# Optimization experiments

Hardware: AMD Instinct MI355X
Metric: run time of the kernel (lower is better)

Reference implementation:

```python
import jax, jax.numpy as jnp
import numpy as np

N_HEAD = 16
D_HEAD = 64
D_MODEL = 1024
SCALE = 1.0 / float(D_HEAD) ** 0.5
LN_EPS = 1e-5


def _rel_shift(x):
    # x: [b, n, i, j] -> Transformer-XL relative shift
    b, n, i, j = x.shape
    x = jnp.pad(x, ((0, 0), (0, 0), (0, 0), (1, 0)))  # zero-pad front of last dim
    x = x.reshape(b, n, j + 1, i)[:, :, 1:, :]
    return x.reshape(b, n, i, j)


def _layer_norm(x, g, b):
    mu = jnp.mean(x, axis=-1, keepdims=True)
    var = jnp.mean(jnp.square(x - mu), axis=-1, keepdims=True)
    return g * (x - mu) / jnp.sqrt(var + LN_EPS) + b


def setup_inputs() -> dict:
    key = jax.random.key(0)
    ks = jax.random.split(key, 8)
    qlen, bsz = 1024, 4
    w = jax.random.normal(ks[0], (qlen, bsz, D_MODEL), jnp.float32)
    r = jax.random.normal(ks[1], (qlen, D_MODEL), jnp.float32)
    r_w_bias = 0.02 * jax.random.normal(ks[2], (N_HEAD, D_HEAD), jnp.float32)
    r_r_bias = 0.02 * jax.random.normal(ks[3], (N_HEAD, D_HEAD), jnp.float32)
    attn_mask = jnp.triu(jnp.ones((qlen, qlen), bool), 1)  # causal, True = masked
    qkv_w = 0.02 * jax.random.normal(ks[4], (D_MODEL, 3 * N_HEAD * D_HEAD), jnp.float32)
    qkv_b = jnp.zeros((3 * N_HEAD * D_HEAD,), jnp.float32)
    rk_w = 0.02 * jax.random.normal(ks[5], (D_MODEL, N_HEAD * D_HEAD), jnp.float32)
    rk_b = jnp.zeros((N_HEAD * D_HEAD,), jnp.float32)
    o_w = 0.02 * jax.random.normal(ks[6], (N_HEAD * D_HEAD, D_MODEL), jnp.float32)
    o_b = jnp.zeros((D_MODEL,), jnp.float32)
    ln_g = jnp.ones((D_MODEL,), jnp.float32)
    ln_b = jnp.zeros((D_MODEL,), jnp.float32)
    return {"w": w, "r": r, "r_w_bias": r_w_bias, "r_r_bias": r_r_bias,
            "qkv_w": qkv_w, "qkv_b": qkv_b, "rk_w": rk_w, "rk_b": rk_b,
            "o_w": o_w, "o_b": o_b, "ln_g": ln_g, "ln_b": ln_b,
            "attn_mask": attn_mask}


def reference(w, r, r_w_bias, r_r_bias, qkv_w, qkv_b, rk_w, rk_b, o_w, o_b, ln_g, ln_b, attn_mask):
    qlen, bsz, _ = w.shape
    # post-lnorm path (pre_lnorm=False)
    heads = w @ qkv_w + qkv_b                       # [q, b, 3*H*D]
    q, k, v = jnp.split(heads, 3, axis=-1)
    q = q.reshape(qlen, bsz, N_HEAD, D_HEAD)
    k = k.reshape(qlen, bsz, N_HEAD, D_HEAD)
    v = v.reshape(qlen, bsz, N_HEAD, D_HEAD)
    rk = (r @ rk_w + rk_b).reshape(-1, N_HEAD, D_HEAD)  # [rlen, H, D]
    AC = jnp.einsum('ibnd,jbnd->bnij', q + r_w_bias, k)
    BD = _rel_shift(jnp.einsum('ibnd,jnd->bnij', q + r_r_bias, rk))
    score = SCALE * (AC + BD)                       # [b, H, q, k]
    score = jnp.where(attn_mask[None, None, :, :], -jnp.inf, score)
    prob = jax.nn.softmax(score, axis=-1)
    vec = jnp.einsum('bnij,jbnd->ibnd', prob, v).reshape(qlen, bsz, N_HEAD * D_HEAD)
    attn_out = vec @ o_w + o_b
    return _layer_norm(w + attn_out, ln_g, ln_b)
```

## Files before the change

### kernel.cpp

```cpp
#include <hip/hip_runtime.h>
#include <math.h>

#define QL 1024
#define BSZ 4
#define NH 16
#define DH 64
#define DM 1024
#define SCALE_F 0.125f

typedef __attribute__((ext_vector_type(8))) short bf16x8;
typedef __attribute__((ext_vector_type(4))) float f32x4;

__device__ __forceinline__ unsigned short f2bf(float f) {
  union { float f; unsigned int u; } c; c.f = f;
  unsigned int u = c.u;
  u += 0x7FFFu + ((u >> 16) & 1u);
  return (unsigned short)(u >> 16);
}
__device__ __forceinline__ float bf2f(unsigned short u) {
  union { unsigned int i; float f; } c; c.i = ((unsigned int)u) << 16;
  return c.f;
}
__device__ __forceinline__ float2 bfp2f(const unsigned short* p) {
  unsigned int u = *(const unsigned int*)p;
  union { unsigned int u; float f; } lo, hi;
  lo.u = (u & 0xFFFFu) << 16;
  hi.u = u & 0xFFFF0000u;
  return make_float2(lo.f, hi.f);
}

__device__ __forceinline__ void ld_lds16(const unsigned short* g, unsigned short* l) {
  __builtin_amdgcn_global_load_lds(
      (const __attribute__((address_space(1))) unsigned int*)g,
      (__attribute__((address_space(3))) unsigned int*)l, 16, 0, 0);
}

__device__ __forceinline__ bf16x8 frag64(const unsigned short* lds, int n, int s) {
  return *(const bf16x8*)(lds + n * 64 + ((s ^ (n & 7)) * 8));
}

__global__ __launch_bounds__(256) void prep_kernel(
    const float* __restrict__ w, const float* __restrict__ r,
    const float* __restrict__ qkv_w, const float* __restrict__ rk_w,
    const float* __restrict__ o_w,
    unsigned short* __restrict__ wb, unsigned short* __restrict__ rb,
    unsigned short* __restrict__ qkv_wt, unsigned short* __restrict__ rk_wt,
    unsigned short* __restrict__ o_wt) {
  __shared__ __align__(16) unsigned short t[64][72];
  const int bid = blockIdx.x, tid = threadIdx.x;
  if (bid < 2560) {
    const float* in = (bid < 2048) ? w : r;
    unsigned short* out = (bid < 2048) ? wb : rb;
    int idx = ((bid < 2048) ? bid : (bid - 2048)) * 256 + tid;
    float4 a = *(const float4*)(in + (size_t)idx * 8);
    float4 b = *(const float4*)(in + (size_t)idx * 8 + 4);
    unsigned short o[8] = {f2bf(a.x), f2bf(a.y), f2bf(a.z), f2bf(a.w),
                           f2bf(b.x), f2bf(b.y), f2bf(b.z), f2bf(b.w)};
    *(uint4*)(out + (size_t)idx * 8) = *(const uint4*)o;
    return;
  }
  const float* in; unsigned short* out; int N, n0, k0;
  if (bid < 3328) {
    int l = bid - 2560; in = qkv_w; out = qkv_wt; N = 3072;
    n0 = (l % 48) * 64; k0 = (l / 48) * 64;
  } else if (bid < 3584) {
    int l = bid - 3328; in = rk_w; out = rk_wt; N = 1024;
    n0 = (l & 15) * 64; k0 = (l >> 4) * 64;
  } else {
    int l = bid - 3584; in = o_w; out = o_wt; N = 1024;
    n0 = (l & 15) * 64; k0 = (l >> 4) * 64;
  }
  for (int f = tid; f < 1024; f += 256) {
    int rr = f >> 4, c4 = (f & 15) * 4;
    float4 v = *(const float4*)(in + (size_t)(k0 + rr) * N + n0 + c4);
    t[c4 + 0][rr] = f2bf(v.x); t[c4 + 1][rr] = f2bf(v.y);
    t[c4 + 2][rr] = f2bf(v.z); t[c4 + 3][rr] = f2bf(v.w);
  }
  __syncthreads();
  for (int f = tid; f < 512; f += 256) {
    int rr = f >> 3, seg = (f & 7) * 8;
    *(uint4*)(out + (size_t)(n0 + rr) * 1024 + k0 + seg) = *(const uint4*)&t[rr][seg];
  }
}

__global__ __launch_bounds__(512) void gemm12(
    const unsigned short* __restrict__ wb, const unsigned short* __restrict__ rb,
    const unsigned short* __restrict__ qkv_wt, const unsigned short* __restrict__ rk_wt,
    const float* __restrict__ qkv_b, const float* __restrict__ rk_b,
    const float* __restrict__ rwb, const float* __restrict__ rrb,
    unsigned short* __restrict__ qbf, unsigned short* __restrict__ kbf,
    unsigned short* __restrict__ vtb, unsigned short* __restrict__ rkbf,
    float* __restrict__ drk) {
  __shared__ __align__(16) unsigned short As[2 * 4096];
  __shared__ __align__(16) unsigned short Bs[2 * 4096];
  const int bid = blockIdx.x, tid = threadIdx.x;
  const int w = tid >> 6, lane = tid & 63;
  const int quad = lane >> 4, l15 = lane & 15;
  const int wr = w >> 2, wc = w & 3;
  const bool job0 = bid < 768;
  const unsigned short *A, *BT;
  const float* bias;
  int bm, bn;
  if (job0) {
    A = wb; BT = qkv_wt; bias = qkv_b;
    bn = (bid % 24) * 128; bm = (bid / 24) * 128;
  } else {
    int l = bid - 768;
    A = rb; BT = rk_wt; bias = rk_b;
    bn = (l & 7) * 128; bm = (l >> 3) * 128;
  }
  const int srow = w * 16 + (lane >> 2);
  const int sseg = (lane & 3) ^ ((lane >> 2) & 3);
  f32x4 acc[4][2] = {};

  auto stage = [&](int bf, int k0) {
    ld_lds16(A + (size_t)(bm + srow) * 1024 + k0 + sseg * 8, As + bf * 4096 + w * 512);
    ld_lds16(BT + (size_t)(bn + srow) * 1024 + k0 + sseg * 8, Bs + bf * 4096 + w * 512);
  };

  int buf = 0;
  stage(0, 0);
  for (int k0 = 0; k0 < 1024; k0 += 32) {
    __syncthreads();
    if (k0 + 32 < 1024) stage(buf ^ 1, k0 + 32);
    const unsigned short* Al = As + buf * 4096;
    const unsigned short* Bl = Bs + buf * 4096;
    const int sa = quad ^ (l15 & 3);
    bf16x8 af[4], bfr[2];
#pragma unroll
    for (int rt = 0; rt < 4; ++rt)
      af[rt] = *(const bf16x8*)&Al[(wr * 64 + rt * 16 + l15) * 32 + sa * 8];
#pragma unroll
    for (int nt = 0; nt < 2; ++nt)
      bfr[nt] = *(const bf16x8*)&Bl[(wc * 32 + nt * 16 + l15) * 32 + sa * 8];
#pragma unroll
    for (int rt = 0; rt < 4; ++rt)
#pragma unroll
      for (int nt = 0; nt < 2; ++nt)
        acc[rt][nt] = __builtin_amdgcn_mfma_f32_16x16x32_bf16(af[rt], bfr[nt], acc[rt][nt], 0, 0, 0);
    buf ^= 1;
  }

  if (job0) {
#pragma unroll
    for (int rt = 0; rt < 4; ++rt)
#pragma unroll
      for (int nt = 0; nt < 2; ++nt) {
        int gc = bn + wc * 32 + nt * 16 + l15;
        float bv = bias[gc];
        int part = gc >> 10, h = (gc >> 6) & 15, d = gc & 63;
#pragma unroll
        for (int reg = 0; reg < 4; ++reg) {
          int gr = bm + wr * 64 + rt * 16 + quad * 4 + reg;
          float val = acc[rt][nt][reg] + bv;
          int i = gr >> 2, b = gr & 3;
          if (part == 0)
            qbf[((size_t)((b * NH + h) * QL + i)) * DH + d] = f2bf(val);
          else if (part == 1)
            kbf[((size_t)((b * NH + h) * QL + i)) * DH + d] = f2bf(val);
          else
            vtb[((size_t)((b * NH + h) * DH + d)) * QL + i] = f2bf(val);
        }
      }
  } else {
    const int h = (bn + wc * 32) >> 6;
    float df[2];
#pragma unroll
    for (int nt = 0; nt < 2; ++nt) {
      int dd = (wc & 1) * 32 + nt * 16 + l15;
      df[nt] = rrb[h * DH + dd] - rwb[h * DH + dd];
    }
#pragma unroll
    for (int rt = 0; rt < 4; ++rt) {
      float s[4] = {0.f, 0.f, 0.f, 0.f};
#pragma unroll
      for (int nt = 0; nt < 2; ++nt) {
        int gc = bn + wc * 32 + nt * 16 + l15;
        float bv = bias[gc];
        int d = gc & 63;
#pragma unroll
        for (int reg = 0; reg < 4; ++reg) {
          int gr = bm + wr * 64 + rt * 16 + quad * 4 + reg;
          float val = acc[rt][nt][reg] + bv;
          rkbf[((size_t)(h * QL + gr)) * DH + d] = f2bf(val);
          s[reg] += val * df[nt];
        }
      }
#pragma unroll
      for (int reg = 0; reg < 4; ++reg) {
        float v = s[reg];
        v += __shfl_xor(v, 1);
        v += __shfl_xor(v, 2);
        v += __shfl_xor(v, 4);
        v += __shfl_xor(v, 8);
        if (l15 == 0) {
          int j = bm + wr * 64 + rt * 16 + quad * 4 + reg;
          atomicAdd(&drk[h * QL + j], v);
        }
      }
    }
  }
}

__global__ __launch_bounds__(512) void gemm_o(
    const unsigned short* __restrict__ A, const unsigned short* __restrict__ BT,
    const float* __restrict__ bias, float* __restrict__ Cf) {
  __shared__ __align__(16) unsigned short As[2 * 4096];
  __shared__ __align__(16) unsigned short Bs[2 * 4096];
  const int tid = threadIdx.x;
  const int w = tid >> 6, lane = tid & 63;
  const int quad = lane >> 4, l15 = lane & 15;
  const int wr = w >> 2, wc = w & 3;
  const int bm = blockIdx.y * 128, bn = blockIdx.x * 128;
  const int srow = w * 16 + (lane >> 2);
  const int sseg = (lane & 3) ^ ((lane >> 2) & 3);
  f32x4 acc[4][2] = {};

  auto stage = [&](int bf, int k0) {
    ld_lds16(A + (size_t)(bm + srow) * 1024 + k0 + sseg * 8, As + bf * 4096 + w * 512);
    ld_lds16(BT + (size_t)(bn + srow) * 1024 + k0 + sseg * 8, Bs + bf * 4096 + w * 512);
  };

  int buf = 0;
  stage(0, 0);
  for (int k0 = 0; k0 < 1024; k0 += 32) {
    __syncthreads();
    if (k0 + 32 < 1024) stage(buf ^ 1, k0 + 32);
    const unsigned short* Al = As + buf * 4096;
    const unsigned short* Bl = Bs + buf * 4096;
    const int sa = quad ^ (l15 & 3);
    bf16x8 af[4], bfr[2];
#pragma unroll
    for (int rt = 0; rt < 4; ++rt)
      af[rt] = *(const bf16x8*)&Al[(wr * 64 + rt * 16 + l15) * 32 + sa * 8];
#pragma unroll
    for (int nt = 0; nt < 2; ++nt)
      bfr[nt] = *(const bf16x8*)&Bl[(wc * 32 + nt * 16 + l15) * 32 + sa * 8];
#pragma unroll
    for (int rt = 0; rt < 4; ++rt)
#pragma unroll
      for (int nt = 0; nt < 2; ++nt)
        acc[rt][nt] = __builtin_amdgcn_mfma_f32_16x16x32_bf16(af[rt], bfr[nt], acc[rt][nt], 0, 0, 0);
    buf ^= 1;
  }

#pragma unroll
  for (int rt = 0; rt < 4; ++rt)
#pragma unroll
    for (int nt = 0; nt < 2; ++nt) {
      int gc = bn + wc * 32 + nt * 16 + l15;
      float bv = bias[gc];
#pragma unroll
      for (int reg = 0; reg < 4; ++reg) {
        int gr = bm + wr * 64 + rt * 16 + quad * 4 + reg;
        Cf[(size_t)gr * DM + gc] = acc[rt][nt][reg] + bv;
      }
    }
}

__global__ __launch_bounds__(256) void attn_kernel(
    const unsigned short* __restrict__ qbf, const unsigned short* __restrict__ kbf,
    const unsigned short* __restrict__ vtb, const unsigned short* __restrict__ rkb,
    const float* __restrict__ drk, const float* __restrict__ rwb,
    unsigned short* __restrict__ vecb) {
  __shared__ __align__(16) unsigned short ks[2 * 4096];
  __shared__ __align__(16) unsigned short vt[2 * 4096];
  __shared__ __align__(16) unsigned short band[2][4096];

  const int tid = threadIdx.x;
  const int w = tid >> 6, lane = tid & 63;
  const int quad = lane >> 4, l15 = lane & 15;
  const int bh = blockIdx.x, b = bh >> 4, h = bh & 15;
  const int yA = blockIdx.y;
  const int i0A = yA * 64, i0B = (15 - yA) * 64;
  const int tA = yA, tB = 15 - yA;

  const unsigned short* kB0 = kbf + (size_t)bh * QL * DH;
  const unsigned short* vB0 = vtb + (size_t)bh * DH * QL;
  const unsigned short* rB0 = rkb + (size_t)h * QL * DH;
  const float* drkh = drk + h * QL;

  const int srow = lane >> 3, sseg = lane & 7;
  auto stage_tile = [&](const unsigned short* gbase, size_t rstride, unsigned short* lds) {
#pragma unroll
    for (int ii = 0; ii < 2; ++ii) {
      int r = ii * 32 + w * 8 + srow;
      int gseg = sseg ^ (r & 7);
      ld_lds16(gbase + (size_t)r * rstride + gseg * 8, lds + ii * 2048 + w * 512);
    }
  };

  auto load_q = [&](int i0, bf16x8* qf) {
    int qrow = i0 + w * 16 + l15;
    const unsigned short* qp = qbf + ((size_t)bh * QL + qrow) * DH;
#pragma unroll
    for (int s = 0; s < 2; ++s) {
      int off = s * 32 + quad * 8;
      uint4 raw = *(const uint4*)(qp + off);
      const unsigned short* ru = (const unsigned short*)&raw;
      float4 wb0 = *(const float4*)(rwb + h * DH + off);
      float4 wb1 = *(const float4*)(rwb + h * DH + off + 4);
      union { bf16x8 v; unsigned short u[8]; } qc;
      qc.u[0] = f2bf(bf2f(ru[0]) + wb0.x); qc.u[1] = f2bf(bf2f(ru[1]) + wb0.y);
      qc.u[2] = f2bf(bf2f(ru[2]) + wb0.z); qc.u[3] = f2bf(bf2f(ru[3]) + wb0.w);
      qc.u[4] = f2bf(bf2f(ru[4]) + wb1.x); qc.u[5] = f2bf(bf2f(ru[5]) + wb1.y);
      qc.u[6] = f2bf(bf2f(ru[6]) + wb1.z); qc.u[7] = f2bf(bf2f(ru[7]) + wb1.w);
      qf[s] = qc.v;
    }
  };
  bf16x8 qfA[2], qfB[2];
  load_q(i0A, qfA);
  load_q(i0B, qfB);

  auto rel_frag = [&](int gb, const bf16x8* qf, f32x4& c, float& dv) {
    int gc = min(gb + l15, QL - 1);
    const unsigned short* rp = rB0 + (size_t)gc * DH;
    f32x4 a = {0.f, 0.f, 0.f, 0.f};
    a = __builtin_amdgcn_mfma_f32_16x16x32_bf16(qf[0], *(const bf16x8*)(rp + quad * 8), a, 0, 0, 0);
    a = __builtin_amdgcn_mfma_f32_16x16x32_bf16(qf[1], *(const bf16x8*)(rp + 32 + quad * 8), a, 0, 0, 0);
    c = a;
    dv = drkh[gc];
  };

  stage_tile(kB0, DH, ks);
  stage_tile(vB0, QL, vt);

  f32x4 raccA[5], raccB[5];
  float dvA[5], dvB[5];
#pragma unroll
  for (int i = 0; i < 5; ++i) {
    rel_frag(1008 - i0A - 16 * w + 16 * i, qfA, raccA[i], dvA[i]);
    rel_frag(1008 - i0B - 16 * w + 16 * i, qfB, raccB[i], dvB[i]);
  }

  float mA[4], lA[4], mB[4], lB[4];
  f32x4 pvA[4], pvB[4];
#pragma unroll
  for (int r = 0; r < 4; ++r) {
    mA[r] = mB[r] = -1e30f; lA[r] = lB[r] = 0.f;
    pvA[r] = pvB[r] = (f32x4){0.f, 0.f, 0.f, 0.f};
  }

  auto do_stream = [&](const bf16x8* qf, f32x4* racc, float* dv, float* mrow, float* lrow,
                       f32x4* pv, bool diag, const unsigned short* ksl,
                       const unsigned short* vtl, unsigned short* bandS) {
    f32x4 sacc[4];
#pragma unroll
    for (int nt = 0; nt < 4; ++nt) {
      int n = nt * 16 + l15;
      f32x4 c = {0.f, 0.f, 0.f, 0.f};
      c = __builtin_amdgcn_mfma_f32_16x16x32_bf16(qf[0], frag64(ksl, n, quad), c, 0, 0, 0);
      c = __builtin_amdgcn_mfma_f32_16x16x32_bf16(qf[1], frag64(ksl, n, 4 + quad), c, 0, 0, 0);
      sacc[nt] = c;
    }
#pragma unroll
    for (int i = 0; i < 5; ++i) {
      float dvv = dv[i];
#pragma unroll
      for (int r = 0; r < 4; ++r) {
        int c = 16 * i + l15 + 4 * quad + r - 15;
        int il = w * 16 + quad * 4 + r;
        if (c >= 0 && c < 64)
          bandS[il * 64 + (c ^ ((il & 7) << 3))] = f2bf(racc[i][r] + dvv);
      }
    }
#pragma unroll
    for (int r = 0; r < 4; ++r) {
      const int il = w * 16 + quad * 4 + r;
      const int sw = (il & 7) << 3;
      float sv[4], smax = -1e30f;
#pragma unroll
      for (int nt = 0; nt < 4; ++nt) {
        int jl = nt * 16 + l15;
        float s = (sacc[nt][r] + bf2f(bandS[il * 64 + (jl ^ sw)])) * SCALE_F;
        if (diag && jl > il) s = -1e30f;
        sv[nt] = s;
        smax = fmaxf(smax, s);
      }
      smax = fmaxf(smax, __shfl_xor(smax, 1));
      smax = fmaxf(smax, __shfl_xor(smax, 2));
      smax = fmaxf(smax, __shfl_xor(smax, 4));
      smax = fmaxf(smax, __shfl_xor(smax, 8));
      float mnew = fmaxf(mrow[r], smax);
      float alpha = __expf(mrow[r] - mnew);
      mrow[r] = mnew;
      float psum = 0.f;
#pragma unroll
      for (int nt = 0; nt < 4; ++nt) {
        float e = __expf(sv[nt] - mnew);
        bandS[il * 64 + ((nt * 16 + l15) ^ sw)] = f2bf(e);
        psum += e;
      }
      psum += __shfl_xor(psum, 1);
      psum += __shfl_xor(psum, 2);
      psum += __shfl_xor(psum, 4);
      psum += __shfl_xor(psum, 8);
      lrow[r] = lrow[r] * alpha + psum;
#pragma unroll
      for (int nt = 0; nt < 4; ++nt) pv[nt][r] *= alpha;
    }
    {
      const int ilr = w * 16 + l15;
      const int swr = ilr & 7;
      bf16x8 pf0 = *(const bf16x8*)&bandS[ilr * 64 + ((quad ^ swr) * 8)];
      bf16x8 pf1 = *(const bf16x8*)&bandS[ilr * 64 + (((4 + quad) ^ swr) * 8)];
#pragma unroll
      for (int nt = 0; nt < 4; ++nt) {
        int n = nt * 16 + l15;
        pv[nt] = __builtin_amdgcn_mfma_f32_16x16x32_bf16(pf0, frag64(vtl, n, quad), pv[nt], 0, 0, 0);
        pv[nt] = __builtin_amdgcn_mfma_f32_16x16x32_bf16(pf1, frag64(vtl, n, 4 + quad), pv[nt], 0, 0, 0);
      }
    }
  };

  int buf = 0;
  for (int t = 0; t <= tB; ++t) {
    __syncthreads();
    if (t < tB) {
      int j1 = (t + 1) << 6;
      stage_tile(kB0 + (size_t)j1 * DH, DH, ks + (buf ^ 1) * 4096);
      stage_tile(vB0 + j1, QL, vt + (buf ^ 1) * 4096);
    }
    const unsigned short* ksl = ks + buf * 4096;
    const unsigned short* vtl = vt + buf * 4096;
    const bool actA = (t <= tA);

    if (t > 0) {
      raccB[0] = raccB[4]; dvB[0] = dvB[4];
      const int GB = 1008 - i0B + 64 * t - 16 * w;
#pragma unroll
      for (int i = 1; i < 5; ++i) rel_frag(GB + 16 * i, qfB, raccB[i], dvB[i]);
      if (actA) {
        raccA[0] = raccA[4]; dvA[0] = dvA[4];
        const int GA = 1008 - i0A + 64 * t - 16 * w;
#pragma unroll
        for (int i = 1; i < 5; ++i) rel_frag(GA + 16 * i, qfA, raccA[i], dvA[i]);
      }
    }

    do_stream(qfB, raccB, dvB, mB, lB, pvB, t == tB, ksl, vtl, band[1]);
    if (actA)
      do_stream(qfA, raccA, dvA, mA, lA, pvA, t == tA, ksl, vtl, band[0]);
    buf ^= 1;
  }

#pragma unroll
  for (int nt = 0; nt < 4; ++nt)
#pragma unroll
    for (int reg = 0; reg < 4; ++reg) {
      int il = w * 16 + quad * 4 + reg;
      int d = nt * 16 + l15;
      vecb[((size_t)((i0A + il) * BSZ + b)) * DM + h * DH + d] = f2bf(pvA[nt][reg] / lA[reg]);
      vecb[((size_t)((i0B + il) * BSZ + b)) * DM + h * DH + d] = f2bf(pvB[nt][reg] / lB[reg]);
    }
}

__global__ __launch_bounds__(256) void ln_kernel(
    const float* __restrict__ w, const float* __restrict__ attn,
    const float* __restrict__ g, const float* __restrict__ bta,
    float* __restrict__ out) {
  __shared__ float red[4];
  __shared__ float sval[2];
  const int row = blockIdx.x, tid = threadIdx.x;
  const float* wr = w + (size_t)row * DM;
  const float* ar = attn + (size_t)row * DM;
  float4 wv = *(const float4*)(wr + tid * 4);
  float4 av = *(const float4*)(ar + tid * 4);
  float x0 = wv.x + av.x, x1 = wv.y + av.y, x2 = wv.z + av.z, x3 = wv.w + av.w;
  float s = x0 + x1 + x2 + x3;
#pragma unroll
  for (int off = 32; off; off >>= 1) s += __shfl_down(s, off, 64);
  const int lane = tid & 63, wvi = tid >> 6;
  if (lane == 0) red[wvi] = s;
  __syncthreads();
  if (tid == 0) sval[0] = (red[0] + red[1] + red[2] + red[3]) * (1.0f / 1024.0f);
  __syncthreads();
  const float mu = sval[0];
  float d0 = x0 - mu, d1 = x1 - mu, d2 = x2 - mu, d3 = x3 - mu;
  float vs2 = d0 * d0 + d1 * d1 + d2 * d2 + d3 * d3;
#pragma unroll
  for (int off = 32; off; off >>= 1) vs2 += __shfl_down(vs2, off, 64);
  if (lane == 0) red[wvi] = vs2;
  __syncthreads();
  if (tid == 0)
    sval[1] = rsqrtf((red[0] + red[1] + red[2] + red[3]) * (1.0f / 1024.0f) + 1e-5f);
  __syncthreads();
  const float inv = sval[1];
  float4 gv = *(const float4*)(g + tid * 4);
  float4 bv = *(const float4*)(bta + tid * 4);
  float4 ov;
  ov.x = gv.x * d0 * inv + bv.x;
  ov.y = gv.y * d1 * inv + bv.y;
  ov.z = gv.z * d2 * inv + bv.z;
  ov.w = gv.w * d3 * inv + bv.w;
  *(float4*)(out + (size_t)row * DM + tid * 4) = ov;
}

extern "C" void kernel_launch(void* const* d_in, const int* in_sizes, int n_in,
                              void* d_out, int out_size, void* d_ws, size_t ws_size,
                              hipStream_t stream) {
  const float* w     = (const float*)d_in[0];
  const float* r     = (const float*)d_in[1];
  const float* rwb   = (const float*)d_in[2];
  const float* rrb   = (const float*)d_in[3];
  const float* qkv_w = (const float*)d_in[4];
  const float* qkv_b = (const float*)d_in[5];
  const float* rk_w  = (const float*)d_in[6];
  const float* rk_b  = (const float*)d_in[7];
  const float* o_w   = (const float*)d_in[8];
  const float* o_b   = (const float*)d_in[9];
  const float* ln_g  = (const float*)d_in[10];
  const float* ln_b  = (const float*)d_in[11];

  float* out = (float*)d_out;
  char* p = (char*)d_ws;
  unsigned short* wb     = (unsigned short*)p; p += (size_t)4096 * 1024 * 2;
  unsigned short* rb     = (unsigned short*)p; p += (size_t)1024 * 1024 * 2;
  unsigned short* qkv_wt = (unsigned short*)p; p += (size_t)3072 * 1024 * 2;
  unsigned short* rk_wt  = (unsigned short*)p; p += (size_t)1024 * 1024 * 2;
  unsigned short* o_wt   = (unsigned short*)p; p += (size_t)1024 * 1024 * 2;
  unsigned short* qbf    = (unsigned short*)p; p += (size_t)BSZ * NH * QL * DH * 2;
  unsigned short* kbf    = (unsigned short*)p; p += (size_t)BSZ * NH * QL * DH * 2;
  unsigned short* vtb    = (unsigned short*)p; p += (size_t)BSZ * NH * QL * DH * 2;
  unsigned short* rkbf   = (unsigned short*)p; p += (size_t)NH * QL * DH * 2;
  float*          drk    = (float*)p;          p += (size_t)NH * QL * 4;
  unsigned short* vecb   = (unsigned short*)p; p += (size_t)4096 * 1024 * 2;
  float*          attnf  = (float*)p;          p += (size_t)4096 * 1024 * 4;

  prep_kernel<<<3840, 256, 0, stream>>>(w, r, qkv_w, rk_w, o_w,
                                        wb, rb, qkv_wt, rk_wt, o_wt);
  hipMemsetAsync(drk, 0, (size_t)NH * QL * 4, stream);
  gemm12<<<832, 512, 0, stream>>>(wb, rb, qkv_wt, rk_wt, qkv_b, rk_b, rwb, rrb,
                                  qbf, kbf, vtb, rkbf, drk);
  attn_kernel<<<dim3(64, 8), 256, 0, stream>>>(qbf, kbf, vtb, rkbf, drk, rwb, vecb);
  gemm_o<<<dim3(8, 32), 512, 0, stream>>>(vecb, o_wt, o_b, attnf);
  ln_kernel<<<4096, 256, 0, stream>>>(w, attnf, ln_g, ln_b, out);
}
```

Baseline: 307.9 us.

## Split attention KV tiles across two wave groups and merge softmax partials

The attention kernel now launches 512 threads: two groups of four waves take alternating key tiles of each query block, and their partial softmax states are merged through LDS at the end. The two query blocks per workgroup are processed one after the other instead of interleaved. The relative-position band is rebuilt with cross-lane shuffles instead of a round trip through LDS, and the row max/sum reductions use DPP. The drk memset is folded into the prep kernel as extra blocks. The aim is more parallel waves and less LDS traffic per tile, at the cost of merge overhead, extra barriers, and a bf16 rounding of one group's partial output.

```diff
diff --git a/kernel.cpp b/kernel.cpp
--- a/kernel.cpp
+++ b/kernel.cpp
@@ -39,15 +39,40 @@
   return *(const bf16x8*)(lds + n * 64 + ((s ^ (n & 7)) * 8));
 }
 
+template <int CTRL>
+__device__ __forceinline__ float dpp_mv(float x) {
+  return __int_as_float(__builtin_amdgcn_update_dpp(
+      0, __float_as_int(x), CTRL, 0xf, 0xf, true));
+}
+__device__ __forceinline__ float rowmax16(float x) {
+  x = fmaxf(x, dpp_mv<0x121>(x));
+  x = fmaxf(x, dpp_mv<0x122>(x));
+  x = fmaxf(x, dpp_mv<0x124>(x));
+  x = fmaxf(x, dpp_mv<0x128>(x));
+  return x;
+}
+__device__ __forceinline__ float rowsum16(float x) {
+  x += dpp_mv<0x121>(x);
+  x += dpp_mv<0x122>(x);
+  x += dpp_mv<0x124>(x);
+  x += dpp_mv<0x128>(x);
+  return x;
+}
+
 __global__ __launch_bounds__(256) void prep_kernel(
     const float* __restrict__ w, const float* __restrict__ r,
     const float* __restrict__ qkv_w, const float* __restrict__ rk_w,
     const float* __restrict__ o_w,
     unsigned short* __restrict__ wb, unsigned short* __restrict__ rb,
     unsigned short* __restrict__ qkv_wt, unsigned short* __restrict__ rk_wt,
-    unsigned short* __restrict__ o_wt) {
+    unsigned short* __restrict__ o_wt, float* __restrict__ drk) {
   __shared__ __align__(16) unsigned short t[64][72];
   const int bid = blockIdx.x, tid = threadIdx.x;
+  if (bid >= 3840) {
+    int idx = (bid - 3840) * 256 + tid;
+    ((float4*)drk)[idx] = make_float4(0.f, 0.f, 0.f, 0.f);
+    return;
+  }
   if (bid < 2560) {
     const float* in = (bid < 2048) ? w : r;
     unsigned short* out = (bid < 2048) ? wb : rb;
@@ -258,201 +283,192 @@
     }
 }
 
-__global__ __launch_bounds__(256) void attn_kernel(
+__global__ __launch_bounds__(512, 4) void attn_kernel(
     const unsigned short* __restrict__ qbf, const unsigned short* __restrict__ kbf,
     const unsigned short* __restrict__ vtb, const unsigned short* __restrict__ rkb,
     const float* __restrict__ drk, const float* __restrict__ rwb,
     unsigned short* __restrict__ vecb) {
-  __shared__ __align__(16) unsigned short ks[2 * 4096];
-  __shared__ __align__(16) unsigned short vt[2 * 4096];
-  __shared__ __align__(16) unsigned short band[2][4096];
+  __shared__ __align__(16) unsigned short SH[40960];
+  unsigned short* Ks = SH;
+  unsigned short* Vs = SH + 16384;
+  unsigned short* PM = SH + 32768;
 
   const int tid = threadIdx.x;
   const int w = tid >> 6, lane = tid & 63;
+  const int g = w >> 2, wg = w & 3;
   const int quad = lane >> 4, l15 = lane & 15;
   const int bh = blockIdx.x, b = bh >> 4, h = bh & 15;
   const int yA = blockIdx.y;
-  const int i0A = yA * 64, i0B = (15 - yA) * 64;
-  const int tA = yA, tB = 15 - yA;
 
   const unsigned short* kB0 = kbf + (size_t)bh * QL * DH;
   const unsigned short* vB0 = vtb + (size_t)bh * DH * QL;
   const unsigned short* rB0 = rkb + (size_t)h * QL * DH;
   const float* drkh = drk + h * QL;
-
-  const int srow = lane >> 3, sseg = lane & 7;
-  auto stage_tile = [&](const unsigned short* gbase, size_t rstride, unsigned short* lds) {
-#pragma unroll
-    for (int ii = 0; ii < 2; ++ii) {
-      int r = ii * 32 + w * 8 + srow;
-      int gseg = sseg ^ (r & 7);
-      ld_lds16(gbase + (size_t)r * rstride + gseg * 8, lds + ii * 2048 + w * 512);
-    }
-  };
-
-  auto load_q = [&](int i0, bf16x8* qf) {
-    int qrow = i0 + w * 16 + l15;
-    const unsigned short* qp = qbf + ((size_t)bh * QL + qrow) * DH;
-#pragma unroll
-    for (int s = 0; s < 2; ++s) {
-      int off = s * 32 + quad * 8;
-      uint4 raw = *(const uint4*)(qp + off);
-      const unsigned short* ru = (const unsigned short*)&raw;
-      float4 wb0 = *(const float4*)(rwb + h * DH + off);
-      float4 wb1 = *(const float4*)(rwb + h * DH + off + 4);
-      union { bf16x8 v; unsigned short u[8]; } qc;
-      qc.u[0] = f2bf(bf2f(ru[0]) + wb0.x); qc.u[1] = f2bf(bf2f(ru[1]) + wb0.y);
-      qc.u[2] = f2bf(bf2f(ru[2]) + wb0.z); qc.u[3] = f2bf(bf2f(ru[3]) + wb0.w);
-      qc.u[4] = f2bf(bf2f(ru[4]) + wb1.x); qc.u[5] = f2bf(bf2f(ru[5]) + wb1.y);
-      qc.u[6] = f2bf(bf2f(ru[6]) + wb1.z); qc.u[7] = f2bf(bf2f(ru[7]) + wb1.w);
-      qf[s] = qc.v;
-    }
-  };
-  bf16x8 qfA[2], qfB[2];
-  load_q(i0A, qfA);
-  load_q(i0B, qfB);
-
-  auto rel_frag = [&](int gb, const bf16x8* qf, f32x4& c, float& dv) {
-    int gc = min(gb + l15, QL - 1);
-    const unsigned short* rp = rB0 + (size_t)gc * DH;
-    f32x4 a = {0.f, 0.f, 0.f, 0.f};
-    a = __builtin_amdgcn_mfma_f32_16x16x32_bf16(qf[0], *(const bf16x8*)(rp + quad * 8), a, 0, 0, 0);
-    a = __builtin_amdgcn_mfma_f32_16x16x32_bf16(qf[1], *(const bf16x8*)(rp + 32 + quad * 8), a, 0, 0, 0);
-    c = a;
-    dv = drkh[gc];
-  };
-
-  stage_tile(kB0, DH, ks);
-  stage_tile(vB0, QL, vt);
-
-  f32x4 raccA[5], raccB[5];
-  float dvA[5], dvB[5];
-#pragma unroll
-  for (int i = 0; i < 5; ++i) {
-    rel_frag(1008 - i0A - 16 * w + 16 * i, qfA, raccA[i], dvA[i]);
-    rel_frag(1008 - i0B - 16 * w + 16 * i, qfB, raccB[i], dvB[i]);
-  }
-
-  float mA[4], lA[4], mB[4], lB[4];
-  f32x4 pvA[4], pvB[4];
-#pragma unroll
-  for (int r = 0; r < 4; ++r) {
-    mA[r] = mB[r] = -1e30f; lA[r] = lB[r] = 0.f;
-    pvA[r] = pvB[r] = (f32x4){0.f, 0.f, 0.f, 0.f};
-  }
-
-  auto do_stream = [&](const bf16x8* qf, f32x4* racc, float* dv, float* mrow, float* lrow,
-                       f32x4* pv, bool diag, const unsigned short* ksl,
-                       const unsigned short* vtl, unsigned short* bandS) {
-    f32x4 sacc[4];
-#pragma unroll
-    for (int nt = 0; nt < 4; ++nt) {
-      int n = nt * 16 + l15;
-      f32x4 c = {0.f, 0.f, 0.f, 0.f};
-      c = __builtin_amdgcn_mfma_f32_16x16x32_bf16(qf[0], frag64(ksl, n, quad), c, 0, 0, 0);
-      c = __builtin_amdgcn_mfma_f32_16x16x32_bf16(qf[1], frag64(ksl, n, 4 + quad), c, 0, 0, 0);
-      sacc[nt] = c;
-    }
-#pragma unroll
-    for (int i = 0; i < 5; ++i) {
-      float dvv = dv[i];
+  unsigned short* pmw = PM + w * 1024;
+  float* ml = (float*)(PM + 4096);
+
+  const int srow8 = lane >> 3, sseg8 = lane & 7;
+
+  for (int stream = 0; stream < 2; ++stream) {
+    const int y = (stream == 0) ? (15 - yA) : yA;
+    const int i0 = y * 64, tS = y;
+    const int np = (tS + 2) >> 1;
+
+    bf16x8 qf[2];
+    {
+      int qrow = i0 + wg * 16 + l15;
+      const unsigned short* qp = qbf + ((size_t)bh * QL + qrow) * DH;
+#pragma unroll
+      for (int s = 0; s < 2; ++s) {
+        int off = s * 32 + quad * 8;
+        uint4 raw = *(const uint4*)(qp + off);
+        const unsigned short* ru = (const unsigned short*)&raw;
+        float4 wb0 = *(const float4*)(rwb + h * DH + off);
+        float4 wb1 = *(const float4*)(rwb + h * DH + off + 4);
+        union { bf16x8 v; unsigned short u[8]; } qc;
+        qc.u[0] = f2bf(bf2f(ru[0]) + wb0.x); qc.u[1] = f2bf(bf2f(ru[1]) + wb0.y);
+        qc.u[2] = f2bf(bf2f(ru[2]) + wb0.z); qc.u[3] = f2bf(bf2f(ru[3]) + wb0.w);
+        qc.u[4] = f2bf(bf2f(ru[4]) + wb1.x); qc.u[5] = f2bf(bf2f(ru[5]) + wb1.y);
+        qc.u[6] = f2bf(bf2f(ru[6]) + wb1.z); qc.u[7] = f2bf(bf2f(ru[7]) + wb1.w);
+        qf[s] = qc.v;
+      }
+    }
+
+    float mrow[4], lrow[4];
+    f32x4 pv[4];
+#pragma unroll
+    for (int r = 0; r < 4; ++r) {
+      mrow[r] = -1e30f; lrow[r] = 0.f;
+      pv[r] = (f32x4){0.f, 0.f, 0.f, 0.f};
+    }
+
+    auto stage_pair = [&](int p, int buf) {
+      int tt = min(2 * p + g, tS);
+      const unsigned short* kb = kB0 + (size_t)(tt * 64) * DH;
+      const unsigned short* vb = vB0 + tt * 64;
+      unsigned short* kd = Ks + buf * 8192 + g * 4096;
+      unsigned short* vd = Vs + buf * 8192 + g * 4096;
+#pragma unroll
+      for (int ii = 0; ii < 2; ++ii) {
+        int row = wg * 16 + ii * 8 + srow8;
+        int gs = sseg8 ^ (row & 7);
+        ld_lds16(kb + (size_t)row * DH + gs * 8, kd + (wg * 16 + ii * 8) * 64);
+        ld_lds16(vb + (size_t)row * QL + gs * 8, vd + (wg * 16 + ii * 8) * 64);
+      }
+    };
+
+    stage_pair(0, 0);
+    for (int p = 0; p < np; ++p) {
+      __syncthreads();
+      if (p + 1 < np) stage_pair(p + 1, (p + 1) & 1);
+      const int t = 2 * p + g;
+      if (t <= tS) {
+        const unsigned short* ksl = Ks + (p & 1) * 8192 + g * 4096;
+        const unsigned short* vsl = Vs + (p & 1) * 8192 + g * 4096;
+        const bool diag = (t == tS);
+
+        f32x4 sacc[4];
+#pragma unroll
+        for (int nt = 0; nt < 4; ++nt) {
+          int n = nt * 16 + l15;
+          f32x4 c = {0.f, 0.f, 0.f, 0.f};
+          c = __builtin_amdgcn_mfma_f32_16x16x32_bf16(qf[0], frag64(ksl, n, quad), c, 0, 0, 0);
+          c = __builtin_amdgcn_mfma_f32_16x16x32_bf16(qf[1], frag64(ksl, n, 4 + quad), c, 0, 0, 0);
+          sacc[nt] = c;
+        }
+
+        const int Bt = 1008 - i0 + 64 * t - 16 * wg;
+        f32x4 rc[5];
+#pragma unroll
+        for (int f = 0; f < 5; ++f) {
+          int row = min(Bt + 16 * f + l15, QL - 1);
+          const unsigned short* rp = rB0 + (size_t)row * DH;
+          f32x4 a = {0.f, 0.f, 0.f, 0.f};
+          a = __builtin_amdgcn_mfma_f32_16x16x32_bf16(qf[0], *(const bf16x8*)(rp + quad * 8), a, 0, 0, 0);
+          a = __builtin_amdgcn_mfma_f32_16x16x32_bf16(qf[1], *(const bf16x8*)(rp + 32 + quad * 8), a, 0, 0, 0);
+          float dv = drkh[row];
+          a[0] += dv; a[1] += dv; a[2] += dv; a[3] += dv;
+          rc[f] = a;
+        }
+
+#pragma unroll
+        for (int r = 0; r < 4; ++r) {
+          const int il = wg * 16 + quad * 4 + r;
+          const int ls = l15 + 15 - quad * 4 - r;
+          const int srcl = (quad << 4) | (ls & 15);
+          float rot[5];
+#pragma unroll
+          for (int f = 0; f < 5; ++f) rot[f] = __shfl(rc[f][r], srcl, 64);
+          const bool lo = ls < 16;
+          float sv[4], mx = -1e30f;
+#pragma unroll
+          for (int nt = 0; nt < 4; ++nt) {
+            float band = lo ? rot[nt] : rot[nt + 1];
+            float s = (sacc[nt][r] + band) * SCALE_F;
+            if (diag && (nt * 16 + l15) > il) s = -1e30f;
+            sv[nt] = s;
+            mx = fmaxf(mx, s);
+          }
+          mx = rowmax16(mx);
+          float mnew = fmaxf(mrow[r], mx);
+          float alpha = __expf(mrow[r] - mnew);
+          mrow[r] = mnew;
+          float psum = 0.f;
+          const int prow = quad * 4 + r;
+          const int psw = prow & 7;
+#pragma unroll
+          for (int nt = 0; nt < 4; ++nt) {
+            float e = __expf(sv[nt] - mnew);
+            psum += e;
+            int jl = nt * 16 + l15;
+            pmw[prow * 64 + (((jl >> 3) ^ psw) << 3) + (jl & 7)] = f2bf(e);
+          }
+          psum = rowsum16(psum);
+          lrow[r] = lrow[r] * alpha + psum;
+#pragma unroll
+          for (int nt = 0; nt < 4; ++nt) pv[nt][r] *= alpha;
+        }
+
+        bf16x8 pf0 = frag64(pmw, l15, quad);
+        bf16x8 pf1 = frag64(pmw, l15, 4 + quad);
+#pragma unroll
+        for (int nt = 0; nt < 4; ++nt) {
+          int n = nt * 16 + l15;
+          pv[nt] = __builtin_amdgcn_mfma_f32_16x16x32_bf16(pf0, frag64(vsl, n, quad), pv[nt], 0, 0, 0);
+          pv[nt] = __builtin_amdgcn_mfma_f32_16x16x32_bf16(pf1, frag64(vsl, n, 4 + quad), pv[nt], 0, 0, 0);
+        }
+      }
+    }
+
+    __syncthreads();
+    if (g == 1) {
 #pragma unroll
       for (int r = 0; r < 4; ++r) {
-        int c = 16 * i + l15 + 4 * quad + r - 15;
-        int il = w * 16 + quad * 4 + r;
-        if (c >= 0 && c < 64)
-          bandS[il * 64 + (c ^ ((il & 7) << 3))] = f2bf(racc[i][r] + dvv);
-      }
-    }
-#pragma unroll
-    for (int r = 0; r < 4; ++r) {
-      const int il = w * 16 + quad * 4 + r;
-      const int sw = (il & 7) << 3;
-      float sv[4], smax = -1e30f;
-#pragma unroll
-      for (int nt = 0; nt < 4; ++nt) {
-        int jl = nt * 16 + l15;
-        float s = (sacc[nt][r] + bf2f(bandS[il * 64 + (jl ^ sw)])) * SCALE_F;
-        if (diag && jl > il) s = -1e30f;
-        sv[nt] = s;
-        smax = fmaxf(smax, s);
-      }
-      smax = fmaxf(smax, __shfl_xor(smax, 1));
-      smax = fmaxf(smax, __shfl_xor(smax, 2));
-      smax = fmaxf(smax, __shfl_xor(smax, 4));
-      smax = fmaxf(smax, __shfl_xor(smax, 8));
-      float mnew = fmaxf(mrow[r], smax);
-      float alpha = __expf(mrow[r] - mnew);
-      mrow[r] = mnew;
-      float psum = 0.f;
-#pragma unroll
-      for (int nt = 0; nt < 4; ++nt) {
-        float e = __expf(sv[nt] - mnew);
-        bandS[il * 64 + ((nt * 16 + l15) ^ sw)] = f2bf(e);
-        psum += e;
-      }
-      psum += __shfl_xor(psum, 1);
-      psum += __shfl_xor(psum, 2);
-      psum += __shfl_xor(psum, 4);
-      psum += __shfl_xor(psum, 8);
-      lrow[r] = lrow[r] * alpha + psum;
-#pragma unroll
-      for (int nt = 0; nt < 4; ++nt) pv[nt][r] *= alpha;
-    }
-    {
-      const int ilr = w * 16 + l15;
-      const int swr = ilr & 7;
-      bf16x8 pf0 = *(const bf16x8*)&bandS[ilr * 64 + ((quad ^ swr) * 8)];
-      bf16x8 pf1 = *(const bf16x8*)&bandS[ilr * 64 + (((4 + quad) ^ swr) * 8)];
-#pragma unroll
-      for (int nt = 0; nt < 4; ++nt) {
-        int n = nt * 16 + l15;
-        pv[nt] = __builtin_amdgcn_mfma_f32_16x16x32_bf16(pf0, frag64(vtl, n, quad), pv[nt], 0, 0, 0);
-        pv[nt] = __builtin_amdgcn_mfma_f32_16x16x32_bf16(pf1, frag64(vtl, n, 4 + quad), pv[nt], 0, 0, 0);
-      }
-    }
-  };
-
-  int buf = 0;
-  for (int t = 0; t <= tB; ++t) {
+        int il = wg * 16 + quad * 4 + r;
+#pragma unroll
+        for (int nt = 0; nt < 4; ++nt)
+          PM[il * 64 + nt * 16 + l15] = f2bf(pv[nt][r]);
+        if (l15 == 0) { ml[il * 2] = mrow[r]; ml[il * 2 + 1] = lrow[r]; }
+      }
+    }
     __syncthreads();
-    if (t < tB) {
-      int j1 = (t + 1) << 6;
-      stage_tile(kB0 + (size_t)j1 * DH, DH, ks + (buf ^ 1) * 4096);
-      stage_tile(vB0 + j1, QL, vt + (buf ^ 1) * 4096);
-    }
-    const unsigned short* ksl = ks + buf * 4096;
-    const unsigned short* vtl = vt + buf * 4096;
-    const bool actA = (t <= tA);
-
-    if (t > 0) {
-      raccB[0] = raccB[4]; dvB[0] = dvB[4];
-      const int GB = 1008 - i0B + 64 * t - 16 * w;
-#pragma unroll
-      for (int i = 1; i < 5; ++i) rel_frag(GB + 16 * i, qfB, raccB[i], dvB[i]);
-      if (actA) {
-        raccA[0] = raccA[4]; dvA[0] = dvA[4];
-        const int GA = 1008 - i0A + 64 * t - 16 * w;
-#pragma unroll
-        for (int i = 1; i < 5; ++i) rel_frag(GA + 16 * i, qfA, raccA[i], dvA[i]);
-      }
-    }
-
-    do_stream(qfB, raccB, dvB, mB, lB, pvB, t == tB, ksl, vtl, band[1]);
-    if (actA)
-      do_stream(qfA, raccA, dvA, mA, lA, pvA, t == tA, ksl, vtl, band[0]);
-    buf ^= 1;
-  }
-
-#pragma unroll
-  for (int nt = 0; nt < 4; ++nt)
-#pragma unroll
-    for (int reg = 0; reg < 4; ++reg) {
-      int il = w * 16 + quad * 4 + reg;
-      int d = nt * 16 + l15;
-      vecb[((size_t)((i0A + il) * BSZ + b)) * DM + h * DH + d] = f2bf(pvA[nt][reg] / lA[reg]);
-      vecb[((size_t)((i0B + il) * BSZ + b)) * DM + h * DH + d] = f2bf(pvB[nt][reg] / lB[reg]);
-    }
+    if (g == 0) {
+#pragma unroll
+      for (int r = 0; r < 4; ++r) {
+        int il = wg * 16 + quad * 4 + r;
+        float m1 = ml[il * 2], l1 = ml[il * 2 + 1];
+        float M = fmaxf(mrow[r], m1);
+        float a0 = __expf(mrow[r] - M), a1 = __expf(m1 - M);
+        float inv = 1.0f / (lrow[r] * a0 + l1 * a1);
+#pragma unroll
+        for (int nt = 0; nt < 4; ++nt) {
+          float pv1 = bf2f(PM[il * 64 + nt * 16 + l15]);
+          float val = (pv[nt][r] * a0 + pv1 * a1) * inv;
+          vecb[((size_t)((i0 + il) * BSZ + b)) * DM + h * DH + nt * 16 + l15] = f2bf(val);
+        }
+      }
+    }
+  }
 }
 
 __global__ __launch_bounds__(256) void ln_kernel(
@@ -527,12 +543,11 @@
   unsigned short* vecb   = (unsigned short*)p; p += (size_t)4096 * 1024 * 2;
   float*          attnf  = (float*)p;          p += (size_t)4096 * 1024 * 4;
 
-  prep_kernel<<<3840, 256, 0, stream>>>(w, r, qkv_w, rk_w, o_w,
-                                        wb, rb, qkv_wt, rk_wt, o_wt);
-  hipMemsetAsync(drk, 0, (size_t)NH * QL * 4, stream);
+  prep_kernel<<<3856, 256, 0, stream>>>(w, r, qkv_w, rk_w, o_w,
+                                        wb, rb, qkv_wt, rk_wt, o_wt, drk);
   gemm12<<<832, 512, 0, stream>>>(wb, rb, qkv_wt, rk_wt, qkv_b, rk_b, rwb, rrb,
                                   qbf, kbf, vtb, rkbf, drk);
-  attn_kernel<<<dim3(64, 8), 256, 0, stream>>>(qbf, kbf, vtb, rkbf, drk, rwb, vecb);
+  attn_kernel<<<dim3(64, 8), 512, 0, stream>>>(qbf, kbf, vtb, rkbf, drk, rwb, vecb);
   gemm_o<<<dim3(8, 32), 512, 0, stream>>>(vecb, o_wt, o_b, attnf);
   ln_kernel<<<4096, 256, 0, stream>>>(w, attnf, ln_g, ln_b, out);
 }
```

New measurement: 304.2 us. Within noise of the previous version (-1.2%).
